# Kernel tuning notes

Measured on AMD Instinct MI355X. Metric: run time of the kernel, lower is better.

Reference implementation:

```python
import jax, jax.numpy as jnp
import numpy as np


def setup_inputs() -> dict:
    key = jax.random.key(0)
    k0, k1, k2, k3, k4 = jax.random.split(key, 5)
    B, S, D, E, H = 2, 4096, 1024, 8, 512
    x = jax.random.normal(k0, (B, S, D), jnp.float32)
    w_router = jax.random.normal(k1, (D, E), jnp.float32) * (D ** -0.5)
    w1 = jax.random.normal(k2, (E, D, H), jnp.float32) * (D ** -0.5)
    w2 = jax.random.normal(k3, (E, H, D), jnp.float32) * (H ** -0.5)
    w3 = jax.random.normal(k4, (E, D, H), jnp.float32) * (D ** -0.5)
    return {"x": x, "w_router": w_router, "w1": w1, "w2": w2, "w3": w3, "top_k": 2}


def reference(x, w_router, w1, w2, w3, top_k):
    """MoE layer: linear router -> softmax -> top_k, then grouped SwiGLU experts
    combined with the routing weights. out = sum_k w_k * Expert_{idx_k}(x)."""
    B, S, D = x.shape
    E = w_router.shape[1]
    xt = x.reshape(-1, D)                              # [T, D]
    T = xt.shape[0]

    # Router
    logits = xt @ w_router                             # [T, E]
    probs = jax.nn.softmax(logits, axis=-1)
    weights, idx = jax.lax.top_k(probs, top_k)         # [T, k], [T, k]

    # Scatter top-k weights into a dense per-token gate over experts.
    gate = jnp.zeros((T, E), xt.dtype).at[jnp.arange(T)[:, None], idx].add(weights)

    h = jax.nn.silu(jnp.einsum('td,edh->teh', xt, w1)) * jnp.einsum('td,edh->teh', xt, w3)
    y = jnp.einsum('te,teh,ehd->td', gate, h, w2)      # combine
    return y.reshape(B, S, D)
```

## Files before the change

### kernel.cpp

```cpp
#include <hip/hip_runtime.h>

#define NT    8192
#define DIM   1024
#define NE    8
#define NH    512
#define NROWS (NT*2)

typedef _Float16 f16;
typedef unsigned int u32;
typedef __attribute__((ext_vector_type(8))) _Float16 f16x8;
typedef __attribute__((ext_vector_type(4))) _Float16 f16x4;
typedef __attribute__((ext_vector_type(2))) _Float16 f16x2;
typedef __attribute__((ext_vector_type(4))) float f32x4;

__device__ __forceinline__ void gl2lds16(const f16* gptr, f16* ldsptr) {
    __builtin_amdgcn_global_load_lds(
        (const __attribute__((address_space(1))) u32*)gptr,
        (__attribute__((address_space(3))) u32*)ldsptr, 16, 0, 0);
}

#define FR(sbuf, row, q) \
    (*(const f16x8*)&sbuf[(row)*32 + (((q) ^ (((row) >> 1) & 3)) << 3)])

#define KC 512
__global__ __launch_bounds__(256) void prep_kernel(
    const float* __restrict__ x, const float* __restrict__ wr,
    const float* __restrict__ w1, const float* __restrict__ w3,
    const float* __restrict__ w2, float* __restrict__ plogits,
    f16* __restrict__ w1t, f16* __restrict__ w3t, f16* __restrict__ w2t)
{
    __shared__ float smem[NE*KC];
    int tid = threadIdx.x;
    int bi = blockIdx.x;
    if (bi < 1024) {
        int bx = bi & 511, by = bi >> 9;
        int kc0 = by * KC;
        for (int i = tid; i < NE*KC; i += 256) {
            int k = i >> 3, e = i & 7;
            smem[e*KC + k] = wr[(size_t)kc0*NE + i];
        }
        __syncthreads();
        int tok = bx*16 + (tid >> 4);
        int kl  = tid & 15;
        float acc[NE];
        #pragma unroll
        for (int e = 0; e < NE; e++) acc[e] = 0.f;
        const float* xrow = x + (size_t)tok*DIM + kc0;
        #pragma unroll
        for (int i = 0; i < KC/64; i++) {
            int kb = i*64 + kl*4;
            float4 xv = *(const float4*)(xrow + kb);
            #pragma unroll
            for (int e = 0; e < NE; e++) {
                float4 wv = *(const float4*)&smem[e*KC + kb];
                acc[e] += xv.x*wv.x + xv.y*wv.y + xv.z*wv.z + xv.w*wv.w;
            }
        }
        #pragma unroll
        for (int e = 0; e < NE; e++) {
            float v = acc[e];
            v += __shfl_xor(v, 1); v += __shfl_xor(v, 2);
            v += __shfl_xor(v, 4); v += __shfl_xor(v, 8);
            acc[e] = v;
        }
        if (kl == 0) {
            float* pp = plogits + ((size_t)by*NT + tok)*NE;
            float4 o0 = {acc[0], acc[1], acc[2], acc[3]};
            float4 o1 = {acc[4], acc[5], acc[6], acc[7]};
            *(float4*)pp = o0;
            *(float4*)(pp + 4) = o1;
        }
    } else {
        int tz = bi - 1024;
        int zx = tz & 511, zy = tz >> 9;
        int tensor = zy >> 3, e = zy & 7;
        const float* src; f16* dst; int R, C;
        if (tensor == 0)      { src = w1; dst = w1t; R = DIM; C = NH; }
        else if (tensor == 1) { src = w3; dst = w3t; R = DIM; C = NH; }
        else                  { src = w2; dst = w2t; R = NH; C = DIM; }
        src += (size_t)e * DIM * NH;
        dst += (size_t)e * DIM * NH;
        int tcols = C >> 5;
        int bx = zx % tcols, by = zx / tcols;
        int r0 = by*32, c0 = bx*32;
        int tx = tid & 31, ty = tid >> 5;
        #pragma unroll
        for (int i = ty; i < 32; i += 8)
            smem[i*33 + tx] = src[(size_t)(r0+i)*C + c0 + tx];
        __syncthreads();
        int p = tid & 15;
        #pragma unroll
        for (int pass = 0; pass < 2; pass++) {
            int i = (tid >> 4) + pass*16;
            f16x2 v = { (f16)smem[(2*p)*33 + i], (f16)smem[(2*p+1)*33 + i] };
            *(f16x2*)&dst[(size_t)(c0+i)*R + r0 + 2*p] = v;
        }
    }
}

__global__ __launch_bounds__(1024) void finalize_kernel(
    const float* __restrict__ plogits, int* __restrict__ tok_ids,
    int* __restrict__ aid, float* __restrict__ row_gate, int* __restrict__ offs)
{
    __shared__ unsigned char s_e[NROWS];
    __shared__ float s_w[NROWS];
    __shared__ int hist[NE], cur[NE];
    int tid = threadIdx.x;
    if (tid < NE) hist[tid] = 0;
    __syncthreads();

    #pragma unroll 1
    for (int it = 0; it < NT/1024; it++) {
        int t = it*1024 + tid;
        const float* p0 = plogits + (size_t)t*NE;
        const float* p1 = plogits + (size_t)NT*NE + (size_t)t*NE;
        float4 a0 = *(const float4*)p0, a1 = *(const float4*)(p0+4);
        float4 b0 = *(const float4*)p1, b1 = *(const float4*)(p1+4);
        float l[NE] = { a0.x+b0.x, a0.y+b0.y, a0.z+b0.z, a0.w+b0.w,
                        a1.x+b1.x, a1.y+b1.y, a1.z+b1.z, a1.w+b1.w };
        float m = l[0];
        #pragma unroll
        for (int e = 1; e < NE; e++) m = fmaxf(m, l[e]);
        float s = 0.f;
        #pragma unroll
        for (int e = 0; e < NE; e++) { l[e] = __expf(l[e] - m); s += l[e]; }
        float inv = 1.f / s;
        int i0 = 0; float v0 = l[0];
        #pragma unroll
        for (int e = 1; e < NE; e++) if (l[e] > v0) { v0 = l[e]; i0 = e; }
        int i1 = -1; float v1 = -1.f;
        #pragma unroll
        for (int e = 0; e < NE; e++) if (e != i0 && l[e] > v1) { v1 = l[e]; i1 = e; }
        s_e[t*2+0] = (unsigned char)i0; s_w[t*2+0] = v0*inv;
        s_e[t*2+1] = (unsigned char)i1; s_w[t*2+1] = v1*inv;
        #pragma unroll
        for (int ee = 0; ee < NE; ee++) {
            int c = __popcll(__ballot(i0 == ee)) + __popcll(__ballot(i1 == ee));
            if ((tid & 63) == 0 && c) atomicAdd(&hist[ee], c);
        }
    }
    __syncthreads();

    if (tid == 0) {
        int s = 0;
        #pragma unroll
        for (int e = 0; e < NE; e++) { offs[e] = s; cur[e] = s; s += hist[e]; }
        offs[NE] = s;
    }
    __syncthreads();

    unsigned long long ltmask = (1ULL << (tid & 63)) - 1;
    #pragma unroll 1
    for (int it = 0; it < NROWS/1024; it++) {
        int id = it*1024 + tid;
        int e = s_e[id];
        int pos = 0;
        #pragma unroll
        for (int ee = 0; ee < NE; ee++) {
            unsigned long long mk = __ballot(e == ee);
            int cnt = __popcll(mk);
            int b = 0;
            if ((tid & 63) == 0 && cnt) b = atomicAdd(&cur[ee], cnt);
            b = __shfl(b, 0);
            if (e == ee) pos = b + __popcll(mk & ltmask);
        }
        tok_ids[pos] = id >> 1;
        aid[pos] = id;
        row_gate[pos] = s_w[id];
    }
}

#define BK 64

#define BM1 64
#define BN1 128
__global__ __launch_bounds__(256,3) void gemm1_kernel(
    const float* __restrict__ x, const int* __restrict__ tok_ids,
    const f16* __restrict__ w1t, const f16* __restrict__ w3t,
    f16* __restrict__ gbuf, const int* __restrict__ offs)
{
    int bi = blockIdx.x;
    int e  = bi & 7;
    int r_ = bi >> 3;
    int nt = r_ & 3;
    int mt = r_ >> 2;
    int off = offs[e];
    int n_e = offs[e+1] - off;
    if (mt*BM1 >= n_e) return;

    __shared__ f16 sA [2][BM1*32];
    __shared__ f16 sB1[2][BN1*32];
    __shared__ f16 sB3[2][BN1*32];
    __shared__ int stok[BM1];

    int tid = threadIdx.x;
    if (tid < BM1) {
        int rloc = mt*BM1 + tid; rloc = rloc < n_e ? rloc : n_e - 1;
        stok[tid] = tok_ids[off + rloc];
    }
    __syncthreads();

    int lane = tid & 63, w = tid >> 6;
    int wcol = w*32;
    int q = lane >> 4, lm = lane & 15;

    int rA = tid >> 2, gA = tid & 3;
    const float* xr = x + (size_t)stok[rA]*DIM + gA*8;
    int pA = (gA ^ ((rA>>1)&3)) << 3;
    f16* sA0p = &sA[0][rA*32 + pA];
    f16* sA1p = &sA[1][rA*32 + pA];

    int lr0 = w*32 + (lane >> 2);
    int lr1 = lr0 + 16;
    int g0 = (lane & 3) ^ ((lr0 >> 1) & 3);
    int g1 = (lane & 3) ^ ((lr1 >> 1) & 3);
    const f16* w1p = w1t + ((size_t)e*NH + nt*BN1)*DIM;
    const f16* w3p = w3t + ((size_t)e*NH + nt*BN1)*DIM;
    const f16* pB1_0 = w1p + (size_t)lr0*DIM + g0*8;
    const f16* pB1_1 = w1p + (size_t)lr1*DIM + g1*8;
    const f16* pB3_0 = w3p + (size_t)lr0*DIM + g0*8;
    const f16* pB3_1 = w3p + (size_t)lr1*DIM + g1*8;
    int lofs0 = lr0*32 + ((lane & 3) << 3);
    int lofs1 = lr1*32 + ((lane & 3) << 3);

    f32x4 acc1[4][2], acc3[4][2];
    #pragma unroll
    for (int a = 0; a < 4; a++)
        #pragma unroll
        for (int b = 0; b < 2; b++) {
            acc1[a][b] = (f32x4){0.f,0.f,0.f,0.f};
            acc3[a][b] = (f32x4){0.f,0.f,0.f,0.f};
        }

    float4 a00 = *(const float4*)(xr);
    float4 a01 = *(const float4*)(xr + 4);
    float4 a10 = *(const float4*)(xr + 32);
    float4 a11 = *(const float4*)(xr + 36);

    for (int k0 = 0; k0 < DIM; k0 += BK) {
        __syncthreads();
        *(f16x8*)sA0p = (f16x8){ (f16)a00.x,(f16)a00.y,(f16)a00.z,(f16)a00.w,
                                 (f16)a01.x,(f16)a01.y,(f16)a01.z,(f16)a01.w };
        *(f16x8*)sA1p = (f16x8){ (f16)a10.x,(f16)a10.y,(f16)a10.z,(f16)a10.w,
                                 (f16)a11.x,(f16)a11.y,(f16)a11.z,(f16)a11.w };
        gl2lds16(pB1_0 + k0,      &sB1[0][lofs0]);
        gl2lds16(pB1_1 + k0,      &sB1[0][lofs1]);
        gl2lds16(pB1_0 + k0 + 32, &sB1[1][lofs0]);
        gl2lds16(pB1_1 + k0 + 32, &sB1[1][lofs1]);
        gl2lds16(pB3_0 + k0,      &sB3[0][lofs0]);
        gl2lds16(pB3_1 + k0,      &sB3[0][lofs1]);
        gl2lds16(pB3_0 + k0 + 32, &sB3[1][lofs0]);
        gl2lds16(pB3_1 + k0 + 32, &sB3[1][lofs1]);
        __syncthreads();
        if (k0 + BK < DIM) {
            a00 = *(const float4*)(xr + k0 + BK);
            a01 = *(const float4*)(xr + k0 + BK + 4);
            a10 = *(const float4*)(xr + k0 + BK + 32);
            a11 = *(const float4*)(xr + k0 + BK + 36);
        }
        #pragma unroll
        for (int ks = 0; ks < 2; ks++) {
            f16x8 aF[4], b1F[2], b3F[2];
            #pragma unroll
            for (int s = 0; s < 4; s++) aF[s] = FR(sA[ks], s*16 + lm, q);
            #pragma unroll
            for (int c = 0; c < 2; c++) {
                b1F[c] = FR(sB1[ks], wcol + c*16 + lm, q);
                b3F[c] = FR(sB3[ks], wcol + c*16 + lm, q);
            }
            #pragma unroll
            for (int sr = 0; sr < 4; sr++)
                #pragma unroll
                for (int sc = 0; sc < 2; sc++) {
                    acc1[sr][sc] = __builtin_amdgcn_mfma_f32_16x16x32_f16(aF[sr], b1F[sc], acc1[sr][sc], 0, 0, 0);
                    acc3[sr][sc] = __builtin_amdgcn_mfma_f32_16x16x32_f16(aF[sr], b3F[sc], acc3[sr][sc], 0, 0, 0);
                }
        }
    }
    #pragma unroll
    for (int sr = 0; sr < 4; sr++) {
        #pragma unroll
        for (int reg = 0; reg < 4; reg++) {
            int row = mt*BM1 + sr*16 + q*4 + reg;
            if (row < n_e) {
                #pragma unroll
                for (int sc = 0; sc < 2; sc++) {
                    int col = nt*BN1 + wcol + sc*16 + lm;
                    float h1 = acc1[sr][sc][reg];
                    float h3 = acc3[sr][sc][reg];
                    float gv = h1 / (1.f + __expf(-h1)) * h3;
                    gbuf[(size_t)(off + row)*NH + col] = (f16)gv;
                }
            }
        }
    }
}

#define BM 128
#define BN 128
__global__ __launch_bounds__(256,3) void gemm2_kernel(
    const f16* __restrict__ gbuf, const f16* __restrict__ w2t,
    const int* __restrict__ offs, const int* __restrict__ aid,
    const float* __restrict__ row_gate, f16* __restrict__ ybuf)
{
    int bi = blockIdx.x;
    int e  = bi & 7;
    int r_ = bi >> 3;
    int nt = r_ & 7;
    int mt = r_ >> 3;
    int off = offs[e];
    int n_e = offs[e+1] - off;
    if (mt*BM >= n_e) return;

    __shared__ f16 sA[2][BM*32];
    __shared__ f16 sB[2][BN*32];
    __shared__ int said[BM];
    __shared__ float sgate[BM];

    int tid = threadIdx.x;
    if (tid < BM) {
        int rloc = mt*BM + tid;
        if (rloc < n_e) { said[tid] = aid[off + rloc]; sgate[tid] = row_gate[off + rloc]; }
        else            { said[tid] = 0; sgate[tid] = 0.f; }
    }

    int lane = tid & 63, w = tid >> 6;
    int wrow = (w >> 1)*64, wcol = (w & 1)*64;
    int q = lane >> 4, lm = lane & 15;

    int lr0 = w*32 + (lane >> 2);
    int lr1 = lr0 + 16;
    int g0 = (lane & 3) ^ ((lr0 >> 1) & 3);
    int g1 = (lane & 3) ^ ((lr1 >> 1) & 3);
    int ga0 = mt*BM + lr0; ga0 = ga0 < n_e ? ga0 : n_e - 1;
    int ga1 = mt*BM + lr1; ga1 = ga1 < n_e ? ga1 : n_e - 1;
    const f16* pA0 = gbuf + (size_t)(off + ga0)*NH + g0*8;
    const f16* pA1 = gbuf + (size_t)(off + ga1)*NH + g1*8;
    const f16* w2p = w2t + ((size_t)e*DIM + nt*BN)*NH;
    const f16* pB0 = w2p + (size_t)lr0*NH + g0*8;
    const f16* pB1 = w2p + (size_t)lr1*NH + g1*8;
    int lofs0 = lr0*32 + ((lane & 3) << 3);
    int lofs1 = lr1*32 + ((lane & 3) << 3);

    f32x4 acc[4][4];
    #pragma unroll
    for (int a = 0; a < 4; a++)
        #pragma unroll
        for (int b = 0; b < 4; b++) acc[a][b] = (f32x4){0.f,0.f,0.f,0.f};

    __syncthreads();

    for (int k0 = 0; k0 < NH; k0 += BK) {
        gl2lds16(pA0 + k0,      &sA[0][lofs0]);
        gl2lds16(pA1 + k0,      &sA[0][lofs1]);
        gl2lds16(pA0 + k0 + 32, &sA[1][lofs0]);
        gl2lds16(pA1 + k0 + 32, &sA[1][lofs1]);
        gl2lds16(pB0 + k0,      &sB[0][lofs0]);
        gl2lds16(pB1 + k0,      &sB[0][lofs1]);
        gl2lds16(pB0 + k0 + 32, &sB[1][lofs0]);
        gl2lds16(pB1 + k0 + 32, &sB[1][lofs1]);
        __syncthreads();
        #pragma unroll
        for (int ks = 0; ks < 2; ks++) {
            f16x8 aF[4], bF[4];
            #pragma unroll
            for (int s = 0; s < 4; s++) {
                aF[s] = FR(sA[ks], wrow + s*16 + lm, q);
                bF[s] = FR(sB[ks], wcol + s*16 + lm, q);
            }
            #pragma unroll
            for (int sr = 0; sr < 4; sr++)
                #pragma unroll
                for (int sc = 0; sc < 4; sc++)
                    acc[sr][sc] = __builtin_amdgcn_mfma_f32_16x16x32_f16(aF[sr], bF[sc], acc[sr][sc], 0, 0, 0);
        }
        __syncthreads();
    }
    #pragma unroll
    for (int sr = 0; sr < 4; sr++) {
        #pragma unroll
        for (int reg = 0; reg < 4; reg++) {
            int lrow = wrow + sr*16 + q*4 + reg;
            if (mt*BM + lrow < n_e) {
                int id = said[lrow];
                float wgt = sgate[lrow];
                #pragma unroll
                for (int sc = 0; sc < 4; sc++) {
                    int col = nt*BN + wcol + sc*16 + lm;
                    ybuf[(size_t)id*DIM + col] = (f16)(wgt * acc[sr][sc][reg]);
                }
            }
        }
    }
}

__global__ __launch_bounds__(256) void combine_kernel(
    const f16* __restrict__ ybuf, float* __restrict__ out)
{
    int gid = blockIdx.x*256 + threadIdx.x;
    int t = gid >> 7;
    int c = (gid & 127) << 3;
    f16x8 y0 = *(const f16x8*)(ybuf + ((size_t)2*t)*DIM + c);
    f16x8 y1 = *(const f16x8*)(ybuf + ((size_t)2*t+1)*DIM + c);
    float* op = out + (size_t)t*DIM + c;
    float4 o0 = { (float)y0[0] + (float)y1[0], (float)y0[1] + (float)y1[1],
                  (float)y0[2] + (float)y1[2], (float)y0[3] + (float)y1[3] };
    float4 o1 = { (float)y0[4] + (float)y1[4], (float)y0[5] + (float)y1[5],
                  (float)y0[6] + (float)y1[6], (float)y0[7] + (float)y1[7] };
    *(float4*)op = o0;
    *(float4*)(op + 4) = o1;
}

extern "C" void kernel_launch(void* const* d_in, const int* in_sizes, int n_in,
                              void* d_out, int out_size, void* d_ws, size_t ws_size,
                              hipStream_t stream)
{
    const float* x  = (const float*)d_in[0];
    const float* wr = (const float*)d_in[1];
    const float* w1 = (const float*)d_in[2];
    const float* w2 = (const float*)d_in[3];
    const float* w3 = (const float*)d_in[4];
    float* out = (float*)d_out;

    char* ws = (char*)d_ws;
    f16* ybuf    = (f16*)ws;        ws += (size_t)NROWS*DIM*sizeof(f16);
    f16* w1t     = (f16*)ws;        ws += (size_t)NE*NH*DIM*sizeof(f16);
    f16* w3t     = (f16*)ws;        ws += (size_t)NE*NH*DIM*sizeof(f16);
    f16* w2t     = (f16*)ws;        ws += (size_t)NE*DIM*NH*sizeof(f16);
    f16* gbuf    = (f16*)ws;        ws += (size_t)NROWS*NH*sizeof(f16);
    float* plogits = (float*)ws;    ws += (size_t)2*NT*NE*4;
    int* tok_ids = (int*)ws;        ws += (size_t)NROWS*4;
    int* aid     = (int*)ws;        ws += (size_t)NROWS*4;
    float* row_gate = (float*)ws;   ws += (size_t)NROWS*4;
    int* offs    = (int*)ws;        ws += 64;
    if (ws_size < (size_t)(ws - (char*)d_ws)) return;

    prep_kernel<<<1024 + 12288, 256, 0, stream>>>(x, wr, w1, w3, w2,
                                                  plogits, w1t, w3t, w2t);
    finalize_kernel<<<1, 1024, 0, stream>>>(plogits, tok_ids, aid, row_gate, offs);
    gemm1_kernel<<<8192, 256, 0, stream>>>(x, tok_ids, w1t, w3t, gbuf, offs);
    gemm2_kernel<<<8192, 256, 0, stream>>>(gbuf, w2t, offs, aid, row_gate, ybuf);
    combine_kernel<<<(NT*(DIM/8))/256, 256, 0, stream>>>(ybuf, out);
}
```

Measured before the change: 270.9 us.

## Pre-convert x to fp16 and double-buffer GEMM K-loops with async LDS prefetch

The prep kernel now also writes an fp16 copy of x into the ybuf workspace. gemm1 can then load its A operand straight into LDS with global_load_lds instead of doing fp32 loads and converting in registers. Both GEMMs are restructured into a double-buffered K loop with BK=32: the next tile is prefetched while the current one is computed, and explicit vmcnt waits and raw barriers replace the earlier load-then-sync pattern. The costs are extra write traffic in prep, reusing ybuf before gemm2 overwrites it, and twice as many loop iterations, each with two barriers.

```diff
diff --git a/kernel.cpp b/kernel.cpp
--- a/kernel.cpp
+++ b/kernel.cpp
@@ -27,6 +27,7 @@
     const float* __restrict__ x, const float* __restrict__ wr,
     const float* __restrict__ w1, const float* __restrict__ w3,
     const float* __restrict__ w2, float* __restrict__ plogits,
+    f16* __restrict__ x16,
     f16* __restrict__ w1t, f16* __restrict__ w3t, f16* __restrict__ w2t)
 {
     __shared__ float smem[NE*KC];
@@ -46,10 +47,13 @@
         #pragma unroll
         for (int e = 0; e < NE; e++) acc[e] = 0.f;
         const float* xrow = x + (size_t)tok*DIM + kc0;
+        f16* xhrow = x16 + (size_t)tok*DIM + kc0;
         #pragma unroll
         for (int i = 0; i < KC/64; i++) {
             int kb = i*64 + kl*4;
             float4 xv = *(const float4*)(xrow + kb);
+            f16x4 xh = { (f16)xv.x, (f16)xv.y, (f16)xv.z, (f16)xv.w };
+            *(f16x4*)(xhrow + kb) = xh;
             #pragma unroll
             for (int e = 0; e < NE; e++) {
                 float4 wv = *(const float4*)&smem[e*KC + kb];
@@ -170,12 +174,13 @@
     }
 }
 
-#define BK 64
 
 #define BM1 64
 #define BN1 128
+#define BK1 32
+#define NK1 (DIM/BK1)
 __global__ __launch_bounds__(256,3) void gemm1_kernel(
-    const float* __restrict__ x, const int* __restrict__ tok_ids,
+    const f16* __restrict__ x16, const int* __restrict__ tok_ids,
     const f16* __restrict__ w1t, const f16* __restrict__ w3t,
     f16* __restrict__ gbuf, const int* __restrict__ offs)
 {
@@ -188,9 +193,9 @@
     int n_e = offs[e+1] - off;
     if (mt*BM1 >= n_e) return;
 
-    __shared__ f16 sA [2][BM1*32];
-    __shared__ f16 sB1[2][BN1*32];
-    __shared__ f16 sB3[2][BN1*32];
+    __shared__ f16 sA [2][BM1*BK1];
+    __shared__ f16 sB1[2][BN1*BK1];
+    __shared__ f16 sB3[2][BN1*BK1];
     __shared__ int stok[BM1];
 
     int tid = threadIdx.x;
@@ -204,24 +209,23 @@
     int wcol = w*32;
     int q = lane >> 4, lm = lane & 15;
 
-    int rA = tid >> 2, gA = tid & 3;
-    const float* xr = x + (size_t)stok[rA]*DIM + gA*8;
-    int pA = (gA ^ ((rA>>1)&3)) << 3;
-    f16* sA0p = &sA[0][rA*32 + pA];
-    f16* sA1p = &sA[1][rA*32 + pA];
-
-    int lr0 = w*32 + (lane >> 2);
-    int lr1 = lr0 + 16;
-    int g0 = (lane & 3) ^ ((lr0 >> 1) & 3);
-    int g1 = (lane & 3) ^ ((lr1 >> 1) & 3);
+    int arow = w*16 + (lane >> 2);
+    int ag   = (lane & 3) ^ ((arow >> 1) & 3);
+    const f16* pa = x16 + (size_t)stok[arow]*DIM + ag*8;
+    const int la = w*512 + lane*8;
+
+    int br0 = w*32 + (lane >> 2);
+    int br1 = br0 + 16;
+    int g0 = (lane & 3) ^ ((br0 >> 1) & 3);
+    int g1 = (lane & 3) ^ ((br1 >> 1) & 3);
     const f16* w1p = w1t + ((size_t)e*NH + nt*BN1)*DIM;
     const f16* w3p = w3t + ((size_t)e*NH + nt*BN1)*DIM;
-    const f16* pB1_0 = w1p + (size_t)lr0*DIM + g0*8;
-    const f16* pB1_1 = w1p + (size_t)lr1*DIM + g1*8;
-    const f16* pB3_0 = w3p + (size_t)lr0*DIM + g0*8;
-    const f16* pB3_1 = w3p + (size_t)lr1*DIM + g1*8;
-    int lofs0 = lr0*32 + ((lane & 3) << 3);
-    int lofs1 = lr1*32 + ((lane & 3) << 3);
+    const f16* pb1_0 = w1p + (size_t)br0*DIM + g0*8;
+    const f16* pb1_1 = w1p + (size_t)br1*DIM + g1*8;
+    const f16* pb3_0 = w3p + (size_t)br0*DIM + g0*8;
+    const f16* pb3_1 = w3p + (size_t)br1*DIM + g1*8;
+    const int lb0 = w*1024 + lane*8;
+    const int lb1 = lb0 + 512;
 
     f32x4 acc1[4][2], acc3[4][2];
     #pragma unroll
@@ -232,50 +236,44 @@
             acc3[a][b] = (f32x4){0.f,0.f,0.f,0.f};
         }
 
-    float4 a00 = *(const float4*)(xr);
-    float4 a01 = *(const float4*)(xr + 4);
-    float4 a10 = *(const float4*)(xr + 32);
-    float4 a11 = *(const float4*)(xr + 36);
-
-    for (int k0 = 0; k0 < DIM; k0 += BK) {
-        __syncthreads();
-        *(f16x8*)sA0p = (f16x8){ (f16)a00.x,(f16)a00.y,(f16)a00.z,(f16)a00.w,
-                                 (f16)a01.x,(f16)a01.y,(f16)a01.z,(f16)a01.w };
-        *(f16x8*)sA1p = (f16x8){ (f16)a10.x,(f16)a10.y,(f16)a10.z,(f16)a10.w,
-                                 (f16)a11.x,(f16)a11.y,(f16)a11.z,(f16)a11.w };
-        gl2lds16(pB1_0 + k0,      &sB1[0][lofs0]);
-        gl2lds16(pB1_1 + k0,      &sB1[0][lofs1]);
-        gl2lds16(pB1_0 + k0 + 32, &sB1[1][lofs0]);
-        gl2lds16(pB1_1 + k0 + 32, &sB1[1][lofs1]);
-        gl2lds16(pB3_0 + k0,      &sB3[0][lofs0]);
-        gl2lds16(pB3_1 + k0,      &sB3[0][lofs1]);
-        gl2lds16(pB3_0 + k0 + 32, &sB3[1][lofs0]);
-        gl2lds16(pB3_1 + k0 + 32, &sB3[1][lofs1]);
-        __syncthreads();
-        if (k0 + BK < DIM) {
-            a00 = *(const float4*)(xr + k0 + BK);
-            a01 = *(const float4*)(xr + k0 + BK + 4);
-            a10 = *(const float4*)(xr + k0 + BK + 32);
-            a11 = *(const float4*)(xr + k0 + BK + 36);
-        }
-        #pragma unroll
-        for (int ks = 0; ks < 2; ks++) {
-            f16x8 aF[4], b1F[2], b3F[2];
+    gl2lds16(pa,    &sA [0][la]);
+    gl2lds16(pb1_0, &sB1[0][lb0]);
+    gl2lds16(pb1_1, &sB1[0][lb1]);
+    gl2lds16(pb3_0, &sB3[0][lb0]);
+    gl2lds16(pb3_1, &sB3[0][lb1]);
+
+    for (int t = 0; t < NK1; t++) {
+        int cur = t & 1, nxt = cur ^ 1;
+        if (t + 1 < NK1) {
+            int k0 = (t+1)*BK1;
+            gl2lds16(pa    + k0, &sA [nxt][la]);
+            gl2lds16(pb1_0 + k0, &sB1[nxt][lb0]);
+            gl2lds16(pb1_1 + k0, &sB1[nxt][lb1]);
+            gl2lds16(pb3_0 + k0, &sB3[nxt][lb0]);
+            gl2lds16(pb3_1 + k0, &sB3[nxt][lb1]);
+            asm volatile("s_waitcnt vmcnt(5)" ::: "memory");
+        } else {
+            asm volatile("s_waitcnt vmcnt(0)" ::: "memory");
+        }
+        __builtin_amdgcn_s_barrier();
+        asm volatile("" ::: "memory");
+        f16x8 aF[4], b1F[2], b3F[2];
+        #pragma unroll
+        for (int s = 0; s < 4; s++) aF[s] = FR(sA[cur], s*16 + lm, q);
+        #pragma unroll
+        for (int c = 0; c < 2; c++) {
+            b1F[c] = FR(sB1[cur], wcol + c*16 + lm, q);
+            b3F[c] = FR(sB3[cur], wcol + c*16 + lm, q);
+        }
+        #pragma unroll
+        for (int sr = 0; sr < 4; sr++)
             #pragma unroll
-            for (int s = 0; s < 4; s++) aF[s] = FR(sA[ks], s*16 + lm, q);
-            #pragma unroll
-            for (int c = 0; c < 2; c++) {
-                b1F[c] = FR(sB1[ks], wcol + c*16 + lm, q);
-                b3F[c] = FR(sB3[ks], wcol + c*16 + lm, q);
+            for (int sc = 0; sc < 2; sc++) {
+                acc1[sr][sc] = __builtin_amdgcn_mfma_f32_16x16x32_f16(aF[sr], b1F[sc], acc1[sr][sc], 0, 0, 0);
+                acc3[sr][sc] = __builtin_amdgcn_mfma_f32_16x16x32_f16(aF[sr], b3F[sc], acc3[sr][sc], 0, 0, 0);
             }
-            #pragma unroll
-            for (int sr = 0; sr < 4; sr++)
-                #pragma unroll
-                for (int sc = 0; sc < 2; sc++) {
-                    acc1[sr][sc] = __builtin_amdgcn_mfma_f32_16x16x32_f16(aF[sr], b1F[sc], acc1[sr][sc], 0, 0, 0);
-                    acc3[sr][sc] = __builtin_amdgcn_mfma_f32_16x16x32_f16(aF[sr], b3F[sc], acc3[sr][sc], 0, 0, 0);
-                }
-        }
+        asm volatile("" ::: "memory");
+        __builtin_amdgcn_s_barrier();
     }
     #pragma unroll
     for (int sr = 0; sr < 4; sr++) {
@@ -298,6 +296,8 @@
 
 #define BM 128
 #define BN 128
+#define BK2 32
+#define NK2 (NH/BK2)
 __global__ __launch_bounds__(256,3) void gemm2_kernel(
     const f16* __restrict__ gbuf, const f16* __restrict__ w2t,
     const int* __restrict__ offs, const int* __restrict__ aid,
@@ -312,8 +312,8 @@
     int n_e = offs[e+1] - off;
     if (mt*BM >= n_e) return;
 
-    __shared__ f16 sA[2][BM*32];
-    __shared__ f16 sB[2][BN*32];
+    __shared__ f16 sA[2][BM*BK2];
+    __shared__ f16 sB[2][BN*BK2];
     __shared__ int said[BM];
     __shared__ float sgate[BM];
 
@@ -323,24 +323,25 @@
         if (rloc < n_e) { said[tid] = aid[off + rloc]; sgate[tid] = row_gate[off + rloc]; }
         else            { said[tid] = 0; sgate[tid] = 0.f; }
     }
+    __syncthreads();
 
     int lane = tid & 63, w = tid >> 6;
     int wrow = (w >> 1)*64, wcol = (w & 1)*64;
     int q = lane >> 4, lm = lane & 15;
 
-    int lr0 = w*32 + (lane >> 2);
-    int lr1 = lr0 + 16;
-    int g0 = (lane & 3) ^ ((lr0 >> 1) & 3);
-    int g1 = (lane & 3) ^ ((lr1 >> 1) & 3);
-    int ga0 = mt*BM + lr0; ga0 = ga0 < n_e ? ga0 : n_e - 1;
-    int ga1 = mt*BM + lr1; ga1 = ga1 < n_e ? ga1 : n_e - 1;
-    const f16* pA0 = gbuf + (size_t)(off + ga0)*NH + g0*8;
-    const f16* pA1 = gbuf + (size_t)(off + ga1)*NH + g1*8;
+    int r0 = w*32 + (lane >> 2);
+    int r1 = r0 + 16;
+    int gA0 = (lane & 3) ^ ((r0 >> 1) & 3);
+    int gA1 = (lane & 3) ^ ((r1 >> 1) & 3);
+    int ga0 = mt*BM + r0; ga0 = ga0 < n_e ? ga0 : n_e - 1;
+    int ga1 = mt*BM + r1; ga1 = ga1 < n_e ? ga1 : n_e - 1;
+    const f16* pa0 = gbuf + (size_t)(off + ga0)*NH + gA0*8;
+    const f16* pa1 = gbuf + (size_t)(off + ga1)*NH + gA1*8;
     const f16* w2p = w2t + ((size_t)e*DIM + nt*BN)*NH;
-    const f16* pB0 = w2p + (size_t)lr0*NH + g0*8;
-    const f16* pB1 = w2p + (size_t)lr1*NH + g1*8;
-    int lofs0 = lr0*32 + ((lane & 3) << 3);
-    int lofs1 = lr1*32 + ((lane & 3) << 3);
+    const f16* pb0 = w2p + (size_t)r0*NH + gA0*8;
+    const f16* pb1 = w2p + (size_t)r1*NH + gA1*8;
+    const int l0 = w*1024 + lane*8;
+    const int l1 = l0 + 512;
 
     f32x4 acc[4][4];
     #pragma unroll
@@ -348,33 +349,38 @@
         #pragma unroll
         for (int b = 0; b < 4; b++) acc[a][b] = (f32x4){0.f,0.f,0.f,0.f};
 
-    __syncthreads();
-
-    for (int k0 = 0; k0 < NH; k0 += BK) {
-        gl2lds16(pA0 + k0,      &sA[0][lofs0]);
-        gl2lds16(pA1 + k0,      &sA[0][lofs1]);
-        gl2lds16(pA0 + k0 + 32, &sA[1][lofs0]);
-        gl2lds16(pA1 + k0 + 32, &sA[1][lofs1]);
-        gl2lds16(pB0 + k0,      &sB[0][lofs0]);
-        gl2lds16(pB1 + k0,      &sB[0][lofs1]);
-        gl2lds16(pB0 + k0 + 32, &sB[1][lofs0]);
-        gl2lds16(pB1 + k0 + 32, &sB[1][lofs1]);
-        __syncthreads();
-        #pragma unroll
-        for (int ks = 0; ks < 2; ks++) {
-            f16x8 aF[4], bF[4];
+    gl2lds16(pa0, &sA[0][l0]);
+    gl2lds16(pa1, &sA[0][l1]);
+    gl2lds16(pb0, &sB[0][l0]);
+    gl2lds16(pb1, &sB[0][l1]);
+
+    for (int t = 0; t < NK2; t++) {
+        int cur = t & 1, nxt = cur ^ 1;
+        if (t + 1 < NK2) {
+            int k0 = (t+1)*BK2;
+            gl2lds16(pa0 + k0, &sA[nxt][l0]);
+            gl2lds16(pa1 + k0, &sA[nxt][l1]);
+            gl2lds16(pb0 + k0, &sB[nxt][l0]);
+            gl2lds16(pb1 + k0, &sB[nxt][l1]);
+            asm volatile("s_waitcnt vmcnt(4)" ::: "memory");
+        } else {
+            asm volatile("s_waitcnt vmcnt(0)" ::: "memory");
+        }
+        __builtin_amdgcn_s_barrier();
+        asm volatile("" ::: "memory");
+        f16x8 aF[4], bF[4];
+        #pragma unroll
+        for (int s = 0; s < 4; s++) {
+            aF[s] = FR(sA[cur], wrow + s*16 + lm, q);
+            bF[s] = FR(sB[cur], wcol + s*16 + lm, q);
+        }
+        #pragma unroll
+        for (int sr = 0; sr < 4; sr++)
             #pragma unroll
-            for (int s = 0; s < 4; s++) {
-                aF[s] = FR(sA[ks], wrow + s*16 + lm, q);
-                bF[s] = FR(sB[ks], wcol + s*16 + lm, q);
-            }
-            #pragma unroll
-            for (int sr = 0; sr < 4; sr++)
-                #pragma unroll
-                for (int sc = 0; sc < 4; sc++)
-                    acc[sr][sc] = __builtin_amdgcn_mfma_f32_16x16x32_f16(aF[sr], bF[sc], acc[sr][sc], 0, 0, 0);
-        }
-        __syncthreads();
+            for (int sc = 0; sc < 4; sc++)
+                acc[sr][sc] = __builtin_amdgcn_mfma_f32_16x16x32_f16(aF[sr], bF[sc], acc[sr][sc], 0, 0, 0);
+        asm volatile("" ::: "memory");
+        __builtin_amdgcn_s_barrier();
     }
     #pragma unroll
     for (int sr = 0; sr < 4; sr++) {
@@ -435,10 +441,12 @@
     int* offs    = (int*)ws;        ws += 64;
     if (ws_size < (size_t)(ws - (char*)d_ws)) return;
 
+    f16* x16 = ybuf;
+
     prep_kernel<<<1024 + 12288, 256, 0, stream>>>(x, wr, w1, w3, w2,
-                                                  plogits, w1t, w3t, w2t);
+                                                  plogits, x16, w1t, w3t, w2t);
     finalize_kernel<<<1, 1024, 0, stream>>>(plogits, tok_ids, aid, row_gate, offs);
-    gemm1_kernel<<<8192, 256, 0, stream>>>(x, tok_ids, w1t, w3t, gbuf, offs);
+    gemm1_kernel<<<8192, 256, 0, stream>>>(x16, tok_ids, w1t, w3t, gbuf, offs);
     gemm2_kernel<<<8192, 256, 0, stream>>>(gbuf, w2t, offs, aid, row_gate, ybuf);
     combine_kernel<<<(NT*(DIM/8))/256, 256, 0, stream>>>(ybuf, out);
 }
```

After: 286.6 us. +5.8%, slower.

## Parallelize routing across blocks and stage fp16 x for async LDS loads in gemm1

Applied to the files above, without the earlier changes.

The single-block finalize kernel is split into a multi-block route kernel, which computes softmax/top-k and a global histogram via atomics, and a multi-block scatter kernel that assigns sorted positions with global atomic cursors. The prep kernel now also writes an fp16 copy of x into the ybuf workspace and zeroes the counters. gemm1 then loads A tiles with global_load_lds directly from that fp16 copy instead of converting fp32 registers. This removes a serial one-block bottleneck and halves the bytes read for gathered A, at the cost of an extra kernel launch and an extra fp16 write of x. Row order inside each expert becomes nondeterministic.

```diff
diff --git a/kernel.cpp b/kernel.cpp
--- a/kernel.cpp
+++ b/kernel.cpp
@@ -27,11 +27,14 @@
     const float* __restrict__ x, const float* __restrict__ wr,
     const float* __restrict__ w1, const float* __restrict__ w3,
     const float* __restrict__ w2, float* __restrict__ plogits,
-    f16* __restrict__ w1t, f16* __restrict__ w3t, f16* __restrict__ w2t)
+    f16* __restrict__ x16,
+    f16* __restrict__ w1t, f16* __restrict__ w3t, f16* __restrict__ w2t,
+    int* __restrict__ zint)
 {
     __shared__ float smem[NE*KC];
     int tid = threadIdx.x;
     int bi = blockIdx.x;
+    if (bi == 0 && tid < 16) zint[tid] = 0;
     if (bi < 1024) {
         int bx = bi & 511, by = bi >> 9;
         int kc0 = by * KC;
@@ -46,10 +49,13 @@
         #pragma unroll
         for (int e = 0; e < NE; e++) acc[e] = 0.f;
         const float* xrow = x + (size_t)tok*DIM + kc0;
+        f16* xhrow = x16 + (size_t)tok*DIM + kc0;
         #pragma unroll
         for (int i = 0; i < KC/64; i++) {
             int kb = i*64 + kl*4;
             float4 xv = *(const float4*)(xrow + kb);
+            f16x4 xh = { (f16)xv.x, (f16)xv.y, (f16)xv.z, (f16)xv.w };
+            *(f16x4*)(xhrow + kb) = xh;
             #pragma unroll
             for (int e = 0; e < NE; e++) {
                 float4 wv = *(const float4*)&smem[e*KC + kb];
@@ -98,84 +104,86 @@
     }
 }
 
-__global__ __launch_bounds__(1024) void finalize_kernel(
-    const float* __restrict__ plogits, int* __restrict__ tok_ids,
-    int* __restrict__ aid, float* __restrict__ row_gate, int* __restrict__ offs)
-{
-    __shared__ unsigned char s_e[NROWS];
-    __shared__ float s_w[NROWS];
-    __shared__ int hist[NE], cur[NE];
+__global__ __launch_bounds__(256) void route_kernel(
+    const float* __restrict__ plogits, unsigned char* __restrict__ ge,
+    float* __restrict__ gw, int* __restrict__ zint)
+{
+    __shared__ int lhist[NE];
     int tid = threadIdx.x;
-    if (tid < NE) hist[tid] = 0;
+    if (tid < NE) lhist[tid] = 0;
     __syncthreads();
 
-    #pragma unroll 1
-    for (int it = 0; it < NT/1024; it++) {
-        int t = it*1024 + tid;
-        const float* p0 = plogits + (size_t)t*NE;
-        const float* p1 = plogits + (size_t)NT*NE + (size_t)t*NE;
-        float4 a0 = *(const float4*)p0, a1 = *(const float4*)(p0+4);
-        float4 b0 = *(const float4*)p1, b1 = *(const float4*)(p1+4);
-        float l[NE] = { a0.x+b0.x, a0.y+b0.y, a0.z+b0.z, a0.w+b0.w,
-                        a1.x+b1.x, a1.y+b1.y, a1.z+b1.z, a1.w+b1.w };
-        float m = l[0];
-        #pragma unroll
-        for (int e = 1; e < NE; e++) m = fmaxf(m, l[e]);
-        float s = 0.f;
-        #pragma unroll
-        for (int e = 0; e < NE; e++) { l[e] = __expf(l[e] - m); s += l[e]; }
-        float inv = 1.f / s;
-        int i0 = 0; float v0 = l[0];
-        #pragma unroll
-        for (int e = 1; e < NE; e++) if (l[e] > v0) { v0 = l[e]; i0 = e; }
-        int i1 = -1; float v1 = -1.f;
-        #pragma unroll
-        for (int e = 0; e < NE; e++) if (e != i0 && l[e] > v1) { v1 = l[e]; i1 = e; }
-        s_e[t*2+0] = (unsigned char)i0; s_w[t*2+0] = v0*inv;
-        s_e[t*2+1] = (unsigned char)i1; s_w[t*2+1] = v1*inv;
-        #pragma unroll
-        for (int ee = 0; ee < NE; ee++) {
-            int c = __popcll(__ballot(i0 == ee)) + __popcll(__ballot(i1 == ee));
-            if ((tid & 63) == 0 && c) atomicAdd(&hist[ee], c);
-        }
+    int t = blockIdx.x*256 + tid;
+    const float* p0 = plogits + (size_t)t*NE;
+    const float* p1 = plogits + (size_t)NT*NE + (size_t)t*NE;
+    float4 a0 = *(const float4*)p0, a1 = *(const float4*)(p0+4);
+    float4 b0 = *(const float4*)p1, b1 = *(const float4*)(p1+4);
+    float l[NE] = { a0.x+b0.x, a0.y+b0.y, a0.z+b0.z, a0.w+b0.w,
+                    a1.x+b1.x, a1.y+b1.y, a1.z+b1.z, a1.w+b1.w };
+    float m = l[0];
+    #pragma unroll
+    for (int e = 1; e < NE; e++) m = fmaxf(m, l[e]);
+    float s = 0.f;
+    #pragma unroll
+    for (int e = 0; e < NE; e++) { l[e] = __expf(l[e] - m); s += l[e]; }
+    float inv = 1.f / s;
+    int i0 = 0; float v0 = l[0];
+    #pragma unroll
+    for (int e = 1; e < NE; e++) if (l[e] > v0) { v0 = l[e]; i0 = e; }
+    int i1 = -1; float v1 = -1.f;
+    #pragma unroll
+    for (int e = 0; e < NE; e++) if (e != i0 && l[e] > v1) { v1 = l[e]; i1 = e; }
+    ge[2*t+0] = (unsigned char)i0; gw[2*t+0] = v0*inv;
+    ge[2*t+1] = (unsigned char)i1; gw[2*t+1] = v1*inv;
+    #pragma unroll
+    for (int ee = 0; ee < NE; ee++) {
+        int c = __popcll(__ballot(i0 == ee)) + __popcll(__ballot(i1 == ee));
+        if ((tid & 63) == 0 && c) atomicAdd(&lhist[ee], c);
     }
     __syncthreads();
-
-    if (tid == 0) {
-        int s = 0;
-        #pragma unroll
-        for (int e = 0; e < NE; e++) { offs[e] = s; cur[e] = s; s += hist[e]; }
+    if (tid < NE && lhist[tid]) atomicAdd(&zint[tid], lhist[tid]);
+}
+
+__global__ __launch_bounds__(256) void scatter_kernel(
+    const unsigned char* __restrict__ ge, const float* __restrict__ gw,
+    int* __restrict__ zint, int* __restrict__ offs, int* __restrict__ tok_ids,
+    int* __restrict__ aid, float* __restrict__ row_gate)
+{
+    const int* ghist = zint;
+    int* gcur = zint + 8;
+    int tid = threadIdx.x;
+    int loffs[NE]; int s = 0;
+    #pragma unroll
+    for (int e = 0; e < NE; e++) { loffs[e] = s; s += ghist[e]; }
+    if (blockIdx.x == 0 && tid == 0) {
+        #pragma unroll
+        for (int e = 0; e < NE; e++) offs[e] = loffs[e];
         offs[NE] = s;
     }
-    __syncthreads();
-
-    unsigned long long ltmask = (1ULL << (tid & 63)) - 1;
-    #pragma unroll 1
-    for (int it = 0; it < NROWS/1024; it++) {
-        int id = it*1024 + tid;
-        int e = s_e[id];
-        int pos = 0;
-        #pragma unroll
-        for (int ee = 0; ee < NE; ee++) {
-            unsigned long long mk = __ballot(e == ee);
-            int cnt = __popcll(mk);
-            int b = 0;
-            if ((tid & 63) == 0 && cnt) b = atomicAdd(&cur[ee], cnt);
-            b = __shfl(b, 0);
-            if (e == ee) pos = b + __popcll(mk & ltmask);
-        }
-        tok_ids[pos] = id >> 1;
-        aid[pos] = id;
-        row_gate[pos] = s_w[id];
-    }
-}
-
-#define BK 64
+    int id = blockIdx.x*256 + tid;
+    int e = ge[id];
+    float wv = gw[id];
+    unsigned long long lt = (1ULL << (tid & 63)) - 1;
+    int pos = 0;
+    #pragma unroll
+    for (int ee = 0; ee < NE; ee++) {
+        unsigned long long mk = __ballot(e == ee);
+        int cnt = __popcll(mk);
+        int b = 0;
+        if ((tid & 63) == 0 && cnt) b = atomicAdd(&gcur[ee], cnt);
+        b = __shfl(b, 0);
+        if (e == ee) pos = loffs[ee] + b + __popcll(mk & lt);
+    }
+    tok_ids[pos] = id >> 1;
+    aid[pos] = id;
+    row_gate[pos] = wv;
+}
+
 
 #define BM1 64
 #define BN1 128
 __global__ __launch_bounds__(256,3) void gemm1_kernel(
-    const float* __restrict__ x, const int* __restrict__ tok_ids,
+    const f16* __restrict__ x16, const int* __restrict__ tok_ids,
     const f16* __restrict__ w1t, const f16* __restrict__ w3t,
     f16* __restrict__ gbuf, const int* __restrict__ offs)
 {
@@ -204,24 +212,23 @@
     int wcol = w*32;
     int q = lane >> 4, lm = lane & 15;
 
-    int rA = tid >> 2, gA = tid & 3;
-    const float* xr = x + (size_t)stok[rA]*DIM + gA*8;
-    int pA = (gA ^ ((rA>>1)&3)) << 3;
-    f16* sA0p = &sA[0][rA*32 + pA];
-    f16* sA1p = &sA[1][rA*32 + pA];
-
-    int lr0 = w*32 + (lane >> 2);
-    int lr1 = lr0 + 16;
-    int g0 = (lane & 3) ^ ((lr0 >> 1) & 3);
-    int g1 = (lane & 3) ^ ((lr1 >> 1) & 3);
+    int arow = w*16 + (lane >> 2);
+    int ag   = (lane & 3) ^ ((arow >> 1) & 3);
+    const f16* pa = x16 + (size_t)stok[arow]*DIM + ag*8;
+    const int la = w*512 + lane*8;
+
+    int br0 = w*32 + (lane >> 2);
+    int br1 = br0 + 16;
+    int g0 = (lane & 3) ^ ((br0 >> 1) & 3);
+    int g1 = (lane & 3) ^ ((br1 >> 1) & 3);
     const f16* w1p = w1t + ((size_t)e*NH + nt*BN1)*DIM;
     const f16* w3p = w3t + ((size_t)e*NH + nt*BN1)*DIM;
-    const f16* pB1_0 = w1p + (size_t)lr0*DIM + g0*8;
-    const f16* pB1_1 = w1p + (size_t)lr1*DIM + g1*8;
-    const f16* pB3_0 = w3p + (size_t)lr0*DIM + g0*8;
-    const f16* pB3_1 = w3p + (size_t)lr1*DIM + g1*8;
-    int lofs0 = lr0*32 + ((lane & 3) << 3);
-    int lofs1 = lr1*32 + ((lane & 3) << 3);
+    const f16* pb1_0 = w1p + (size_t)br0*DIM + g0*8;
+    const f16* pb1_1 = w1p + (size_t)br1*DIM + g1*8;
+    const f16* pb3_0 = w3p + (size_t)br0*DIM + g0*8;
+    const f16* pb3_1 = w3p + (size_t)br1*DIM + g1*8;
+    const int lofs0 = br0*32 + ((lane & 3) << 3);
+    const int lofs1 = br1*32 + ((lane & 3) << 3);
 
     f32x4 acc1[4][2], acc3[4][2];
     #pragma unroll
@@ -232,32 +239,19 @@
             acc3[a][b] = (f32x4){0.f,0.f,0.f,0.f};
         }
 
-    float4 a00 = *(const float4*)(xr);
-    float4 a01 = *(const float4*)(xr + 4);
-    float4 a10 = *(const float4*)(xr + 32);
-    float4 a11 = *(const float4*)(xr + 36);
-
-    for (int k0 = 0; k0 < DIM; k0 += BK) {
-        __syncthreads();
-        *(f16x8*)sA0p = (f16x8){ (f16)a00.x,(f16)a00.y,(f16)a00.z,(f16)a00.w,
-                                 (f16)a01.x,(f16)a01.y,(f16)a01.z,(f16)a01.w };
-        *(f16x8*)sA1p = (f16x8){ (f16)a10.x,(f16)a10.y,(f16)a10.z,(f16)a10.w,
-                                 (f16)a11.x,(f16)a11.y,(f16)a11.z,(f16)a11.w };
-        gl2lds16(pB1_0 + k0,      &sB1[0][lofs0]);
-        gl2lds16(pB1_1 + k0,      &sB1[0][lofs1]);
-        gl2lds16(pB1_0 + k0 + 32, &sB1[1][lofs0]);
-        gl2lds16(pB1_1 + k0 + 32, &sB1[1][lofs1]);
-        gl2lds16(pB3_0 + k0,      &sB3[0][lofs0]);
-        gl2lds16(pB3_1 + k0,      &sB3[0][lofs1]);
-        gl2lds16(pB3_0 + k0 + 32, &sB3[1][lofs0]);
-        gl2lds16(pB3_1 + k0 + 32, &sB3[1][lofs1]);
-        __syncthreads();
-        if (k0 + BK < DIM) {
-            a00 = *(const float4*)(xr + k0 + BK);
-            a01 = *(const float4*)(xr + k0 + BK + 4);
-            a10 = *(const float4*)(xr + k0 + BK + 32);
-            a11 = *(const float4*)(xr + k0 + BK + 36);
-        }
+    for (int k0 = 0; k0 < DIM; k0 += 64) {
+        __syncthreads();
+        gl2lds16(pa + k0,         &sA [0][la]);
+        gl2lds16(pa + k0 + 32,    &sA [1][la]);
+        gl2lds16(pb1_0 + k0,      &sB1[0][lofs0]);
+        gl2lds16(pb1_1 + k0,      &sB1[0][lofs1]);
+        gl2lds16(pb1_0 + k0 + 32, &sB1[1][lofs0]);
+        gl2lds16(pb1_1 + k0 + 32, &sB1[1][lofs1]);
+        gl2lds16(pb3_0 + k0,      &sB3[0][lofs0]);
+        gl2lds16(pb3_1 + k0,      &sB3[0][lofs1]);
+        gl2lds16(pb3_0 + k0 + 32, &sB3[1][lofs0]);
+        gl2lds16(pb3_1 + k0 + 32, &sB3[1][lofs1]);
+        __syncthreads();
         #pragma unroll
         for (int ks = 0; ks < 2; ks++) {
             f16x8 aF[4], b1F[2], b3F[2];
@@ -339,8 +333,8 @@
     const f16* w2p = w2t + ((size_t)e*DIM + nt*BN)*NH;
     const f16* pB0 = w2p + (size_t)lr0*NH + g0*8;
     const f16* pB1 = w2p + (size_t)lr1*NH + g1*8;
-    int lofs0 = lr0*32 + ((lane & 3) << 3);
-    int lofs1 = lr1*32 + ((lane & 3) << 3);
+    const int lofs0 = lr0*32 + ((lane & 3) << 3);
+    const int lofs1 = lr1*32 + ((lane & 3) << 3);
 
     f32x4 acc[4][4];
     #pragma unroll
@@ -350,7 +344,7 @@
 
     __syncthreads();
 
-    for (int k0 = 0; k0 < NH; k0 += BK) {
+    for (int k0 = 0; k0 < NH; k0 += 64) {
         gl2lds16(pA0 + k0,      &sA[0][lofs0]);
         gl2lds16(pA1 + k0,      &sA[0][lofs1]);
         gl2lds16(pA0 + k0 + 32, &sA[1][lofs0]);
@@ -433,12 +427,19 @@
     int* aid     = (int*)ws;        ws += (size_t)NROWS*4;
     float* row_gate = (float*)ws;   ws += (size_t)NROWS*4;
     int* offs    = (int*)ws;        ws += 64;
+    unsigned char* ge = (unsigned char*)ws; ws += (size_t)NROWS;
+    float* gw    = (float*)ws;      ws += (size_t)NROWS*4;
+    int* zint    = (int*)ws;        ws += 64;
     if (ws_size < (size_t)(ws - (char*)d_ws)) return;
 
+    f16* x16 = ybuf;
+
     prep_kernel<<<1024 + 12288, 256, 0, stream>>>(x, wr, w1, w3, w2,
-                                                  plogits, w1t, w3t, w2t);
-    finalize_kernel<<<1, 1024, 0, stream>>>(plogits, tok_ids, aid, row_gate, offs);
-    gemm1_kernel<<<8192, 256, 0, stream>>>(x, tok_ids, w1t, w3t, gbuf, offs);
+                                                  plogits, x16, w1t, w3t, w2t, zint);
+    route_kernel<<<NT/256, 256, 0, stream>>>(plogits, ge, gw, zint);
+    scatter_kernel<<<NROWS/256, 256, 0, stream>>>(ge, gw, zint, offs,
+                                                  tok_ids, aid, row_gate);
+    gemm1_kernel<<<8192, 256, 0, stream>>>(x16, tok_ids, w1t, w3t, gbuf, offs);
     gemm2_kernel<<<8192, 256, 0, stream>>>(gbuf, w2t, offs, aid, row_gate, ybuf);
     combine_kernel<<<(NT*(DIM/8))/256, 256, 0, stream>>>(ybuf, out);
 }
```

Result: no change. 270.6 us (-0.1%).
